# Kernel optimization log

Hardware: AMD Instinct MI355X
Metric: run time of the kernel (lower is better)

Reference implementation:

```python
import jax, jax.numpy as jnp
import numpy as np

N_NODES = 100000
N_EDGES = 1600000
IN_DIM, HID, OUT_DIM = 8, 64, 32
LN_EPS = 1e-5


def _layer_norm(x, g, b):
    m = jnp.mean(x, axis=-1, keepdims=True)
    v = jnp.var(x, axis=-1, keepdims=True)
    return g * (x - m) / jnp.sqrt(v + LN_EPS) + b


def _gat(h, W, a, src, dst, n_nodes):
    # Wh: [N, H]
    Wh = h @ W
    # per-edge score: dot(Wh[src], Wh[dst]) * sum(a)  (leaky relu, slope 0.2)
    s = jnp.sum(Wh[src] * Wh[dst], axis=-1)  # [E]
    e = jax.nn.leaky_relu(s * jnp.sum(a), negative_slope=0.2)
    att = jax.nn.softmax(e)  # NOTE: global softmax over ALL edges, as in source
    msg = att[:, None] * Wh[src]  # [E, H]
    h_prime = jax.ops.segment_sum(msg, dst, num_segments=n_nodes)
    return jax.nn.elu(h_prime)


def _stack(x, src, dst, params):
    out = x
    for (W, a, g, b) in params:
        out = _layer_norm(_gat(out, W, a, src, dst, N_NODES), g, b)
    return out


def setup_inputs() -> dict:
    key = jax.random.key(0)
    ks = jax.random.split(key, 24)
    d = {}
    d['x'] = jax.random.normal(ks[0], (N_NODES, IN_DIM), dtype=jnp.float32)
    d['edge_index'] = jax.random.randint(ks[1], (2, N_EDGES), 0, N_NODES, dtype=jnp.int32)
    d['edge_type'] = jax.random.randint(ks[2], (N_EDGES,), 0, 2, dtype=jnp.int32)
    d['temporal_edge_index'] = jax.random.randint(ks[3], (2, N_EDGES), 0, N_NODES, dtype=jnp.int32)

    def xavier(k, shape):
        fan_in, fan_out = shape[0], shape[1]
        lim = float(np.sqrt(6.0 / (fan_in + fan_out)))
        return jax.random.uniform(k, shape, jnp.float32, -lim, lim)

    i = 4
    for pfx in ('s', 't'):
        for li, ind in enumerate((IN_DIM, HID)):
            d[f'{pfx}W{li}'] = xavier(ks[i], (ind, HID)); i += 1
            d[f'{pfx}a{li}'] = xavier(ks[i], (2 * HID, 1)); i += 1
            d[f'{pfx}g{li}'] = jnp.ones((HID,), jnp.float32)
            d[f'{pfx}b{li}'] = jnp.zeros((HID,), jnp.float32)
    d['cW1'] = xavier(ks[i], (HID, OUT_DIM)); i += 1
    d['cb1'] = jnp.zeros((OUT_DIM,), jnp.float32)
    d['cW2'] = xavier(ks[i], (OUT_DIM, 1)); i += 1
    d['cb2'] = jnp.zeros((1,), jnp.float32)
    return d


def reference(x, edge_index, edge_type, temporal_edge_index,
              sW0, sa0, sg0, sb0, sW1, sa1, sg1, sb1,
              tW0, ta0, tg0, tb0, tW1, ta1, tg1, tb1,
              cW1, cb1, cW2, cb2):
    sp = _stack(x, edge_index[0], edge_index[1],
                [(sW0, sa0, sg0, sb0), (sW1, sa1, sg1, sb1)])
    tp = _stack(x, temporal_edge_index[0], temporal_edge_index[1],
                [(tW0, ta0, tg0, tb0), (tW1, ta1, tg1, tb1)])
    h = sp + tp
    h = jax.nn.relu(h @ cW1 + cb1)
    return jax.nn.sigmoid(h @ cW2 + cb2)  # [N, 1]
```

## Files before the change

### kernel.cpp

```cpp
#include <hip/hip_runtime.h>
#include <math.h>

#define NN 100000
#define NE 1600000
#define HID 64
#define NBE 2048
#define NBG 2048
#define NBF 2048
#define EPB 2048
#define NBLK 782
#define NBUCK 98
#define MATN (2 * NBUCK * NBLK)
#define ESHIFT 30.0f

__global__ void prep4(const float* __restrict__ a0, const float* __restrict__ a1,
                      const float* __restrict__ a2, const float* __restrict__ a3,
                      float* __restrict__ sum_a) {
    int w = threadIdx.x >> 6, lane = threadIdx.x & 63;
    const float* a = (w == 0) ? a0 : (w == 1) ? a1 : (w == 2) ? a2 : a3;
    float v = a[lane] + a[lane + 64];
    #pragma unroll
    for (int o = 32; o >= 1; o >>= 1) v += __shfl_xor(v, o);
    if (lane == 0) sum_a[w] = v;
}

__global__ void bucket_hist(const int* __restrict__ eiS, const int* __restrict__ eiT,
                            int* __restrict__ cnt) {
    __shared__ int hist[NBUCK];
    int t = threadIdx.x;
    int side = blockIdx.x >= NBLK;
    int blk = blockIdx.x - side * NBLK;
    const int* dst = (side ? eiT : eiS) + NE;
    if (t < NBUCK) hist[t] = 0;
    __syncthreads();
    int base = blk * EPB;
    #pragma unroll
    for (int k = 0; k < EPB / 256; k++) {
        int e = base + k * 256 + t;
        if (e < NE) atomicAdd(&hist[dst[e] >> 10], 1);
    }
    __syncthreads();
    if (t < NBUCK) cnt[side * (NBUCK * NBLK) + t * NBLK + blk] = hist[t];
}

__global__ void scanA(const int* __restrict__ deg, int* __restrict__ rowtmp,
                      int* __restrict__ bsum, int n) {
    __shared__ int sh[256];
    int t = threadIdx.x;
    int base = blockIdx.x * 1024 + t * 4;
    int a0 = (base + 0 < n) ? deg[base + 0] : 0;
    int a1 = (base + 1 < n) ? deg[base + 1] : 0;
    int a2 = (base + 2 < n) ? deg[base + 2] : 0;
    int a3 = (base + 3 < n) ? deg[base + 3] : 0;
    int s = a0 + a1 + a2 + a3;
    sh[t] = s;
    __syncthreads();
    for (int off = 1; off < 256; off <<= 1) {
        int x = (t >= off) ? sh[t - off] : 0;
        __syncthreads();
        sh[t] += x;
        __syncthreads();
    }
    int excl = sh[t] - s;
    if (t == 255) bsum[blockIdx.x] = sh[255];
    if (base + 0 < n) rowtmp[base + 0] = excl;
    if (base + 1 < n) rowtmp[base + 1] = excl + a0;
    if (base + 2 < n) rowtmp[base + 2] = excl + a0 + a1;
    if (base + 3 < n) rowtmp[base + 3] = excl + a0 + a1 + a2;
}

__global__ void scanB(int* __restrict__ bsum, int nb) {
    __shared__ int sh[256];
    int t = threadIdx.x;
    int v = (t < nb) ? bsum[t] : 0;
    sh[t] = v;
    __syncthreads();
    for (int off = 1; off < 256; off <<= 1) {
        int x = (t >= off) ? sh[t - off] : 0;
        __syncthreads();
        sh[t] += x;
        __syncthreads();
    }
    if (t < nb) bsum[t] = sh[t] - v;
}

__global__ void scanC(const int* __restrict__ rowtmp, const int* __restrict__ bsum,
                      int* __restrict__ outp, int n, int total) {
    int i = blockIdx.x * 256 + threadIdx.x;
    if (i < n) outp[i] = rowtmp[i] + bsum[i >> 10];
    if (i == n) outp[n] = total;
}

__global__ void bucket_scatter(const int* __restrict__ eiS, const int* __restrict__ eiT,
                               const int* __restrict__ off, int2* __restrict__ part) {
    __shared__ int cur[NBUCK];
    int t = threadIdx.x;
    int side = blockIdx.x >= NBLK;
    int blk = blockIdx.x - side * NBLK;
    const int* ei = side ? eiT : eiS;
    if (t < NBUCK) cur[t] = off[side * (NBUCK * NBLK) + t * NBLK + blk];
    __syncthreads();
    int base = blk * EPB;
    #pragma unroll
    for (int k = 0; k < EPB / 256; k++) {
        int e = base + k * 256 + t;
        if (e < NE) {
            int s = ei[e], d = ei[NE + e];
            int p = atomicAdd(&cur[d >> 10], 1);
            part[p] = make_int2(s, d);
        }
    }
}

__global__ void bucket_csr(const int2* __restrict__ part, const int* __restrict__ off,
                           int* __restrict__ rowptrS, int* __restrict__ rowptrT,
                           int* __restrict__ csrsS, int* __restrict__ csrsT) {
    __shared__ int hist[1024];
    __shared__ int sh[1024];
    int t = threadIdx.x;
    int g = blockIdx.x;
    int side = g >= NBUCK;
    int bin = g - side * NBUCK;
    int start = off[g * NBLK];
    int end = off[(g + 1) * NBLK];
    hist[t] = 0;
    __syncthreads();
    for (int i = start + t; i < end; i += 1024)
        atomicAdd(&hist[part[i].y & 1023], 1);
    __syncthreads();
    int own = hist[t];
    sh[t] = own;
    __syncthreads();
    for (int o = 1; o < 1024; o <<= 1) {
        int x = (t >= o) ? sh[t - o] : 0;
        __syncthreads();
        sh[t] += x;
        __syncthreads();
    }
    int excl = sh[t] - own;
    int node = bin * 1024 + t;
    int* rowptr = side ? rowptrT : rowptrS;
    if (node < NN) rowptr[node] = (start - side * NE) + excl;
    if (t == 0 && bin == NBUCK - 1) rowptr[NN] = NE;
    __syncthreads();
    hist[t] = start + excl;
    __syncthreads();
    int* csr = side ? csrsT : csrsS;
    int sub = side * NE;
    for (int i = start + t; i < end; i += 1024) {
        int2 e = part[i];
        int p = atomicAdd(&hist[e.y & 1023], 1);
        csr[p - sub] = e.x;
    }
}

__global__ void gemm2_k8(const float* __restrict__ x, const float* __restrict__ WS,
                         const float* __restrict__ WT, float* __restrict__ WhS,
                         float* __restrict__ WhT, int n) {
    const int nbh = (NN + 63) / 64;
    int side = blockIdx.x >= nbh;
    int blk = blockIdx.x - side * nbh;
    const float* W = side ? WT : WS;
    float* Wh = side ? WhT : WhS;
    __shared__ float Wl[8][HID];
    int t = threadIdx.x;
    for (int i = t; i < 8 * HID / 4; i += 256)
        ((float4*)Wl)[i] = ((const float4*)W)[i];
    __syncthreads();
    int node = blk * 64 + (t >> 2);
    int c0 = (t & 3) * 16;
    if (node >= n) return;
    float acc[16];
    #pragma unroll
    for (int j = 0; j < 16; j++) acc[j] = 0.f;
    const float* hr = x + (size_t)node * 8;
    #pragma unroll
    for (int k4 = 0; k4 < 2; k4++) {
        float4 hv = *(const float4*)(hr + k4 * 4);
        #pragma unroll
        for (int j = 0; j < 16; j++)
            acc[j] += hv.x * Wl[k4*4+0][c0+j] + hv.y * Wl[k4*4+1][c0+j]
                    + hv.z * Wl[k4*4+2][c0+j] + hv.w * Wl[k4*4+3][c0+j];
    }
    float* o = Wh + (size_t)node * HID + c0;
    #pragma unroll
    for (int j = 0; j < 16; j += 4)
        *(float4*)(o + j) = make_float4(acc[j], acc[j+1], acc[j+2], acc[j+3]);
}

__global__ void edge_agg2(const float* __restrict__ WhS, const float* __restrict__ WhT,
                          const int* __restrict__ rowptrS, const int* __restrict__ rowptrT,
                          const int* __restrict__ csrsS, const int* __restrict__ csrsT,
                          const float* __restrict__ sum_a, int aiS, int aiT,
                          float* __restrict__ accS, float* __restrict__ accT,
                          float* __restrict__ bsumz, int n) {
    int side = blockIdx.x >= NBE;
    int blk = blockIdx.x - side * NBE;
    const float* Wh = side ? WhT : WhS;
    const int* rowptr = side ? rowptrT : rowptrS;
    const int* csrs = side ? csrsT : csrsS;
    float* acc = side ? accT : accS;
    float sa = sum_a[side ? aiT : aiS];
    int t = threadIdx.x;
    int w = t >> 6, lane = t & 63;
    int g = lane >> 3, l8 = lane & 7;
    float Zw = 0.f;
    for (int node = blk * 4 + w; node < n; node += NBE * 4) {
        const float* qp = Wh + (size_t)node * HID + l8 * 8;
        float4 q0 = *(const float4*)qp, q1 = *(const float4*)(qp + 4);
        int beg = rowptr[node], end = rowptr[node + 1];
        float z = 0.f;
        float4 a0 = make_float4(0,0,0,0), a1 = make_float4(0,0,0,0);
        for (int i = beg; i < end; i += 8) {
            int idx = i + g;
            bool act = idx < end;
            int s = csrs[act ? idx : beg];
            const float* vp = Wh + (size_t)s * HID + l8 * 8;
            float4 v0 = *(const float4*)vp, v1 = *(const float4*)(vp + 4);
            float x = q0.x*v0.x + q0.y*v0.y + q0.z*v0.z + q0.w*v0.w
                    + q1.x*v1.x + q1.y*v1.y + q1.z*v1.z + q1.w*v1.w;
            x += __shfl_xor(x, 1); x += __shfl_xor(x, 2); x += __shfl_xor(x, 4);
            float e = x * sa;
            e = e > 0.f ? e : 0.2f * e;
            float wg = act ? __expf(e - ESHIFT) : 0.f;
            z += wg;
            a0.x += wg*v0.x; a0.y += wg*v0.y; a0.z += wg*v0.z; a0.w += wg*v0.w;
            a1.x += wg*v1.x; a1.y += wg*v1.y; a1.z += wg*v1.z; a1.w += wg*v1.w;
        }
        #pragma unroll
        for (int o = 8; o <= 32; o <<= 1) {
            z    += __shfl_xor(z, o);
            a0.x += __shfl_xor(a0.x, o); a0.y += __shfl_xor(a0.y, o);
            a0.z += __shfl_xor(a0.z, o); a0.w += __shfl_xor(a0.w, o);
            a1.x += __shfl_xor(a1.x, o); a1.y += __shfl_xor(a1.y, o);
            a1.z += __shfl_xor(a1.z, o); a1.w += __shfl_xor(a1.w, o);
        }
        if (g == 0) {
            float* ap = acc + (size_t)node * HID + l8 * 8;
            *(float4*)ap = a0; *(float4*)(ap + 4) = a1;
        }
        Zw += z;
    }
    __shared__ float shz[4];
    if (lane == 0) shz[w] = Zw;
    __syncthreads();
    if (t == 0) bsumz[blockIdx.x] = (shz[0] + shz[1]) + (shz[2] + shz[3]);
}

__device__ __forceinline__ float combine_invZ(const float* __restrict__ bsumz,
                                              int base, float* shred) {
    int t = threadIdx.x;
    float lz = 0.f;
    for (int i = t; i < NBE; i += 256) lz += bsumz[base + i];
    #pragma unroll
    for (int o = 32; o >= 1; o >>= 1) lz += __shfl_xor(lz, o);
    if ((t & 63) == 0) shred[t >> 6] = lz;
    __syncthreads();
    float Zt = (shred[0] + shred[1]) + (shred[2] + shred[3]);
    __syncthreads();
    return 1.f / Zt;
}

__global__ void normgemm2(const float* __restrict__ accS, const float* __restrict__ accT,
                          const float* __restrict__ bsumz,
                          const float* __restrict__ gS, const float* __restrict__ bS,
                          const float* __restrict__ gT, const float* __restrict__ bT,
                          const float* __restrict__ W1S, const float* __restrict__ W1T,
                          float* __restrict__ WhS, float* __restrict__ WhT, int n) {
    int side = blockIdx.x >= NBG;
    int blk = blockIdx.x - side * NBG;
    const float* acc = side ? accT : accS;
    const float* g = side ? gT : gS;
    const float* b = side ? bT : bS;
    const float* W1 = side ? W1T : W1S;
    float* Wh = side ? WhT : WhS;
    __shared__ float shred[4];
    float invZ = combine_invZ(bsumz, side * NBE, shred);
    __shared__ float Wl[64 * 64];
    int t = threadIdx.x;
    for (int i = t; i < 1024; i += 256)
        ((float4*)Wl)[i] = ((const float4*)W1)[i];
    __syncthreads();
    __shared__ float hrow[4][64];
    int w = t >> 6, lane = t & 63;
    float gl = g[lane], bl = b[lane];
    for (int node = blk * 4 + w; node < n; node += NBG * 4) {
        float v = acc[(size_t)node * HID + lane] * invZ;
        v = v > 0.f ? v : expm1f(v);
        float s = v, s2 = v * v;
        #pragma unroll
        for (int o = 32; o >= 1; o >>= 1) {
            s += __shfl_xor(s, o);
            s2 += __shfl_xor(s2, o);
        }
        float mean = s * (1.f / 64.f);
        float var = s2 * (1.f / 64.f) - mean * mean;
        float hn = gl * (v - mean) * rsqrtf(var + 1e-5f) + bl;
        hrow[w][lane] = hn;
        float o2 = 0.f;
        #pragma unroll
        for (int k = 0; k < 64; k++) o2 += hrow[w][k] * Wl[k * 64 + lane];
        Wh[(size_t)node * HID + lane] = o2;
    }
}

__global__ void normfinal(const float* __restrict__ accS, const float* __restrict__ accT,
                          const float* __restrict__ bsumz,
                          const float* __restrict__ gS, const float* __restrict__ bS,
                          const float* __restrict__ gT, const float* __restrict__ bT,
                          const float* __restrict__ cW1, const float* __restrict__ cb1,
                          const float* __restrict__ cW2, const float* __restrict__ cb2,
                          float* __restrict__ out, int n) {
    __shared__ float shred[4];
    float invZS = combine_invZ(bsumz, 0, shred);
    float invZT = combine_invZ(bsumz, NBE, shred);
    __shared__ float W1l[64 * 32];
    __shared__ float W2l[32], B1l[32];
    int t = threadIdx.x;
    for (int i = t; i < 512; i += 256)
        ((float4*)W1l)[i] = ((const float4*)cW1)[i];
    if (t < 32) { W2l[t] = cW2[t]; B1l[t] = cb1[t]; }
    __syncthreads();
    float c2 = cb2[0];
    __shared__ float hrow[4][64];
    int w = t >> 6, lane = t & 63;
    int j = lane & 31;
    float glS = gS[lane], blS = bS[lane], glT = gT[lane], blT = bT[lane];
    for (int node = blockIdx.x * 4 + w; node < n; node += NBF * 4) {
        float vS = accS[(size_t)node * HID + lane] * invZS;
        vS = vS > 0.f ? vS : expm1f(vS);
        float sA = vS, sB = vS * vS;
        #pragma unroll
        for (int o = 32; o >= 1; o >>= 1) { sA += __shfl_xor(sA, o); sB += __shfl_xor(sB, o); }
        float meanS = sA * (1.f / 64.f);
        float varS = sB * (1.f / 64.f) - meanS * meanS;
        float hS = glS * (vS - meanS) * rsqrtf(varS + 1e-5f) + blS;
        float vT = accT[(size_t)node * HID + lane] * invZT;
        vT = vT > 0.f ? vT : expm1f(vT);
        sA = vT; sB = vT * vT;
        #pragma unroll
        for (int o = 32; o >= 1; o >>= 1) { sA += __shfl_xor(sA, o); sB += __shfl_xor(sB, o); }
        float meanT = sA * (1.f / 64.f);
        float varT = sB * (1.f / 64.f) - meanT * meanT;
        float hT = glT * (vT - meanT) * rsqrtf(varT + 1e-5f) + blT;
        hrow[w][lane] = hS + hT;
        float a = B1l[j];
        #pragma unroll
        for (int k = 0; k < 64; k++) a += hrow[w][k] * W1l[k * 32 + j];
        a = fmaxf(a, 0.f);
        float p = a * W2l[j];
        #pragma unroll
        for (int o = 16; o >= 1; o >>= 1) p += __shfl_xor(p, o, 32);
        if (lane == 0) out[node] = 1.f / (1.f + expf(-(p + c2)));
    }
}

extern "C" void kernel_launch(void* const* d_in, const int* in_sizes, int n_in,
                              void* d_out, int out_size, void* d_ws, size_t ws_size,
                              hipStream_t stream) {
    const float* x   = (const float*)d_in[0];
    const int*   ei  = (const int*)d_in[1];
    const int*   tei = (const int*)d_in[3];
    const float* sW0 = (const float*)d_in[4],  *sa0 = (const float*)d_in[5];
    const float* sg0 = (const float*)d_in[6],  *sb0 = (const float*)d_in[7];
    const float* sW1 = (const float*)d_in[8],  *sa1 = (const float*)d_in[9];
    const float* sg1 = (const float*)d_in[10], *sb1 = (const float*)d_in[11];
    const float* tW0 = (const float*)d_in[12], *ta0 = (const float*)d_in[13];
    const float* tg0 = (const float*)d_in[14], *tb0 = (const float*)d_in[15];
    const float* tW1 = (const float*)d_in[16], *ta1 = (const float*)d_in[17];
    const float* tg1 = (const float*)d_in[18], *tb1 = (const float*)d_in[19];
    const float* cW1 = (const float*)d_in[20], *cb1 = (const float*)d_in[21];
    const float* cW2 = (const float*)d_in[22], *cb2 = (const float*)d_in[23];
    float* out = (float*)d_out;

    float* ws = (float*)d_ws;
    size_t o = 0;
    float* hS  = ws + o; o += (size_t)NN * HID;
    float* hT  = ws + o; o += (size_t)NN * HID;
    float* WhS = ws + o; o += (size_t)NN * HID;
    float* WhT = ws + o; o += (size_t)NN * HID;
    float* bsumz = ws + o; o += 2 * NBE;
    float* sum_a = ws + o; o += 4;
    int* ip = (int*)(ws + o);
    int* rowptrS = ip; ip += NN + 1;
    int* rowptrT = ip; ip += NN + 1;
    int* csrsS   = ip; ip += NE;
    int* csrsT   = ip; ip += NE;

    int2* part   = (int2*)WhS;
    int*  cnt    = (int*)WhT;
    int*  offm   = cnt + (MATN + 1);
    int*  rowtmp = offm + (MATN + 1);
    int*  bsum   = rowtmp + MATN;

    const int NSB = (MATN + 1023) / 1024;

    bucket_hist<<<2 * NBLK, 256, 0, stream>>>(ei, tei, cnt);
    scanA<<<NSB, 256, 0, stream>>>(cnt, rowtmp, bsum, MATN);
    scanB<<<1, 256, 0, stream>>>(bsum, NSB);
    scanC<<<(MATN + 256) / 256, 256, 0, stream>>>(rowtmp, bsum, offm, MATN, 2 * NE);
    bucket_scatter<<<2 * NBLK, 256, 0, stream>>>(ei, tei, offm, part);
    bucket_csr<<<2 * NBUCK, 1024, 0, stream>>>(part, offm, rowptrS, rowptrT, csrsS, csrsT);

    prep4<<<1, 256, 0, stream>>>(sa0, sa1, ta0, ta1, sum_a);

    const int nbh = (NN + 63) / 64;

    gemm2_k8<<<2 * nbh, 256, 0, stream>>>(x, sW0, tW0, WhS, WhT, NN);
    edge_agg2<<<2 * NBE, 256, 0, stream>>>(WhS, WhT, rowptrS, rowptrT, csrsS, csrsT,
                                           sum_a, 0, 2, hS, hT, bsumz, NN);
    normgemm2<<<2 * NBG, 256, 0, stream>>>(hS, hT, bsumz,
                                           sg0, sb0, tg0, tb0, sW1, tW1, WhS, WhT, NN);
    edge_agg2<<<2 * NBE, 256, 0, stream>>>(WhS, WhT, rowptrS, rowptrT, csrsS, csrsT,
                                           sum_a, 1, 3, hS, hT, bsumz, NN);
    normfinal<<<NBF, 256, 0, stream>>>(hS, hT, bsumz,
                                       sg1, sb1, tg1, tb1, cW1, cb1, cW2, cb2, out, NN);
}
```

Measured before the change: 465.8 us.

## Unroll edge loop by two, chunk contiguous nodes per wave, fold prep4 into scanB

Each wavefront now handles a contiguous chunk of 13 nodes. It loads their row pointers in one go and broadcasts them with shuffles instead of reading rowptr per node. The edge loop handles 16 neighbours per iteration, two independent gathers in flight, to give more memory-level parallelism before falling back to the 8-wide masked tail. The separate prep4 launch is merged into scanB to save one kernel launch. Chunked assignment may cause load imbalance because node degrees vary.

```diff
diff --git a/kernel.cpp b/kernel.cpp
--- a/kernel.cpp
+++ b/kernel.cpp
@@ -7,22 +7,12 @@
 #define NBE 2048
 #define NBG 2048
 #define NBF 2048
+#define CHUNK 13
 #define EPB 2048
 #define NBLK 782
 #define NBUCK 98
 #define MATN (2 * NBUCK * NBLK)
 #define ESHIFT 30.0f
-
-__global__ void prep4(const float* __restrict__ a0, const float* __restrict__ a1,
-                      const float* __restrict__ a2, const float* __restrict__ a3,
-                      float* __restrict__ sum_a) {
-    int w = threadIdx.x >> 6, lane = threadIdx.x & 63;
-    const float* a = (w == 0) ? a0 : (w == 1) ? a1 : (w == 2) ? a2 : a3;
-    float v = a[lane] + a[lane + 64];
-    #pragma unroll
-    for (int o = 32; o >= 1; o >>= 1) v += __shfl_xor(v, o);
-    if (lane == 0) sum_a[w] = v;
-}
 
 __global__ void bucket_hist(const int* __restrict__ eiS, const int* __restrict__ eiT,
                             int* __restrict__ cnt) {
@@ -69,7 +59,10 @@
     if (base + 3 < n) rowtmp[base + 3] = excl + a0 + a1 + a2;
 }
 
-__global__ void scanB(int* __restrict__ bsum, int nb) {
+__global__ void scanB(int* __restrict__ bsum, int nb,
+                      const float* __restrict__ a0, const float* __restrict__ a1,
+                      const float* __restrict__ a2, const float* __restrict__ a3,
+                      float* __restrict__ sum_a) {
     __shared__ int sh[256];
     int t = threadIdx.x;
     int v = (t < nb) ? bsum[t] : 0;
@@ -82,6 +75,12 @@
         __syncthreads();
     }
     if (t < nb) bsum[t] = sh[t] - v;
+    int w = t >> 6, lane = t & 63;
+    const float* a = (w == 0) ? a0 : (w == 1) ? a1 : (w == 2) ? a2 : a3;
+    float av = a[lane] + a[lane + 64];
+    #pragma unroll
+    for (int o = 32; o >= 1; o >>= 1) av += __shfl_xor(av, o);
+    if (lane == 0) sum_a[w] = av;
 }
 
 __global__ void scanC(const int* __restrict__ rowtmp, const int* __restrict__ bsum,
@@ -204,17 +203,47 @@
     int t = threadIdx.x;
     int w = t >> 6, lane = t & 63;
     int g = lane >> 3, l8 = lane & 7;
+    int base = (blk * 4 + w) * CHUNK;
+    int lim = min(base + CHUNK, n);
+    int rp = rowptr[min(base + min(lane, CHUNK), n)];
     float Zw = 0.f;
-    for (int node = blk * 4 + w; node < n; node += NBE * 4) {
+    for (int node = base; node < lim; ++node) {
+        int kk = node - base;
+        int beg = __shfl(rp, kk);
+        int end = __shfl(rp, kk + 1);
         const float* qp = Wh + (size_t)node * HID + l8 * 8;
         float4 q0 = *(const float4*)qp, q1 = *(const float4*)(qp + 4);
-        int beg = rowptr[node], end = rowptr[node + 1];
         float z = 0.f;
         float4 a0 = make_float4(0,0,0,0), a1 = make_float4(0,0,0,0);
-        for (int i = beg; i < end; i += 8) {
+        int i = beg;
+        for (; i + 16 <= end; i += 16) {
+            int sA = csrs[i + g];
+            int sB = csrs[i + 8 + g];
+            const float* vpA = Wh + (size_t)sA * HID + l8 * 8;
+            const float* vpB = Wh + (size_t)sB * HID + l8 * 8;
+            float4 vA0 = *(const float4*)vpA, vA1 = *(const float4*)(vpA + 4);
+            float4 vB0 = *(const float4*)vpB, vB1 = *(const float4*)(vpB + 4);
+            float xA = q0.x*vA0.x + q0.y*vA0.y + q0.z*vA0.z + q0.w*vA0.w
+                     + q1.x*vA1.x + q1.y*vA1.y + q1.z*vA1.z + q1.w*vA1.w;
+            float xB = q0.x*vB0.x + q0.y*vB0.y + q0.z*vB0.z + q0.w*vB0.w
+                     + q1.x*vB1.x + q1.y*vB1.y + q1.z*vB1.z + q1.w*vB1.w;
+            xA += __shfl_xor(xA, 1); xB += __shfl_xor(xB, 1);
+            xA += __shfl_xor(xA, 2); xB += __shfl_xor(xB, 2);
+            xA += __shfl_xor(xA, 4); xB += __shfl_xor(xB, 4);
+            float eA = xA * sa, eB = xB * sa;
+            eA = eA > 0.f ? eA : 0.2f * eA;
+            eB = eB > 0.f ? eB : 0.2f * eB;
+            float wA = __expf(eA - ESHIFT), wB = __expf(eB - ESHIFT);
+            z += wA + wB;
+            a0.x += wA*vA0.x + wB*vB0.x; a0.y += wA*vA0.y + wB*vB0.y;
+            a0.z += wA*vA0.z + wB*vB0.z; a0.w += wA*vA0.w + wB*vB0.w;
+            a1.x += wA*vA1.x + wB*vB1.x; a1.y += wA*vA1.y + wB*vB1.y;
+            a1.z += wA*vA1.z + wB*vB1.z; a1.w += wA*vA1.w + wB*vB1.w;
+        }
+        for (; i < end; i += 8) {
             int idx = i + g;
             bool act = idx < end;
-            int s = csrs[act ? idx : beg];
+            int s = csrs[act ? idx : end - 1];
             const float* vp = Wh + (size_t)s * HID + l8 * 8;
             float4 v0 = *(const float4*)vp, v1 = *(const float4*)(vp + 4);
             float x = q0.x*v0.x + q0.y*v0.y + q0.z*v0.z + q0.w*v0.w
@@ -397,12 +426,10 @@
 
     bucket_hist<<<2 * NBLK, 256, 0, stream>>>(ei, tei, cnt);
     scanA<<<NSB, 256, 0, stream>>>(cnt, rowtmp, bsum, MATN);
-    scanB<<<1, 256, 0, stream>>>(bsum, NSB);
+    scanB<<<1, 256, 0, stream>>>(bsum, NSB, sa0, sa1, ta0, ta1, sum_a);
     scanC<<<(MATN + 256) / 256, 256, 0, stream>>>(rowtmp, bsum, offm, MATN, 2 * NE);
     bucket_scatter<<<2 * NBLK, 256, 0, stream>>>(ei, tei, offm, part);
     bucket_csr<<<2 * NBUCK, 1024, 0, stream>>>(part, offm, rowptrS, rowptrT, csrsS, csrsT);
-
-    prep4<<<1, 256, 0, stream>>>(sa0, sa1, ta0, ta1, sum_a);
 
     const int nbh = (NN + 63) / 64;
 
```

Result: slower. 505.2 us (+8.5%).
